# Performance work log

Measured on AMD Instinct MI355X. Metric: run time of the kernel, lower is better.

Reference implementation:

```python
import jax, jax.numpy as jnp
import numpy as np

T, B, N = 512, 256, 128


def setup_inputs() -> dict:
    key = jax.random.key(0)
    k1, k2, k3, k4, k5, k6 = jax.random.split(key, 6)
    emit = jax.random.normal(k1, (T, B, N), dtype=jnp.float32)
    target = jax.random.randint(k2, (T, B), 0, N)
    # prefix-true mask from random lengths in [1, T]
    lengths = jax.random.randint(k3, (B,), 1, T + 1)
    mask = jnp.arange(T)[:, None] < lengths[None, :]
    std = (1.0 / N) ** 0.5
    trans = jax.random.normal(k4, (N, N), dtype=jnp.float32) * std
    strans = jax.random.normal(k5, (N,), dtype=jnp.float32) * std
    etrans = jax.random.normal(k6, (N,), dtype=jnp.float32) * std
    return {"emit": emit, "target": target, "mask": mask,
            "trans": trans, "strans": strans, "etrans": etrans}


def _logZ(emit, mask, trans, strans, etrans):
    alpha0 = strans + emit[0]  # (B, N)

    def step(alpha, xs):
        e_t, m_t = xs  # (B, N), (B,)
        # scores[b, j] = logsumexp_i(alpha[b, i] + trans[i, j] + e_t[b, j])
        scores = jax.scipy.special.logsumexp(
            alpha[:, :, None] + trans[None, :, :] + e_t[:, None, :], axis=1)
        alpha = jnp.where(m_t[:, None], scores, alpha)
        return alpha, None

    alpha, _ = jax.lax.scan(step, alpha0, (emit[1:], mask[1:]))
    return jax.scipy.special.logsumexp(alpha + etrans, axis=1).sum()


def _score(emit, target, mask, trans, strans, etrans):
    Tn, Bn, _ = emit.shape
    # emission scores of gold tags: (T, B)
    sc = jnp.take_along_axis(emit, target[:, :, None], axis=2)[..., 0]
    # transition scores between consecutive gold tags
    sc = sc.at[1:].add(trans[target[:-1], target[1:]])
    score = jnp.sum(jnp.where(mask, sc, jnp.float32(0.0)))
    ends = mask.astype(jnp.int32).sum(axis=0) - 1  # (B,)
    score = score + strans[target[0]].sum()
    score = score + etrans[target[ends, jnp.arange(Bn)]].sum()
    return score


def reference(emit, target, mask, trans, strans, etrans):
    Bn = emit.shape[1]
    logZ = _logZ(emit, mask, trans, strans, etrans)
    score = _score(emit, target, mask, trans, strans, etrans)
    return (logZ - score) / Bn
```

## Files before the change

### kernel.cpp

```cpp
#include <hip/hip_runtime.h>

#define TT 512
#define BB 256
#define NN 128
#define MW 16
#define NWG (BB / MW)
#define STH 144

#define LENS_OFF 256
#define AF_OFF 2048
#define CF_OFF (AF_OFF + BB * NN * 4)
#define BU_OFF (CF_OFF + 1024)
#define CB_OFF (BU_OFF + BB * NN * 4)
#define WS_NEED ((size_t)CB_OFF + 1024)

typedef __attribute__((ext_vector_type(8))) short short8_t;
typedef __attribute__((ext_vector_type(4))) float f32x4;

__device__ __forceinline__ unsigned short f2bf(float f) {
  unsigned u = __float_as_uint(f);
  return (unsigned short)((u + 0x7FFF + ((u >> 16) & 1)) >> 16);
}
__device__ __forceinline__ float bf2f(unsigned short h) {
  return __uint_as_float(((unsigned)h) << 16);
}
__device__ __forceinline__ int orig_j(int p) {
  return 32 * (p >> 5) + 16 * (p & 1) + ((p >> 1) & 15);
}
__device__ __forceinline__ unsigned pk_bf16(float a, float b) {
  unsigned r;
  asm("v_cvt_pk_bf16_f32 %0, %1, %2" : "=v"(r) : "v"(a), "v"(b));
  return r;
}

#define BARRIER_LGKM() \
  asm volatile("s_waitcnt lgkmcnt(0)\n\ts_barrier" ::: "memory")

template <bool FWD>
__device__ __forceinline__ void step_one(
    int T_, bool NORM, const float* __restrict__ emit,
    unsigned short (&sVg)[2][MW * STH], int (&nrmg)[2][MW], int& nb,
    int (&cloc)[4], const int (&lm1)[4], const int (&off8)[8],
    float (&RL)[8], const float (&RO)[8], float (&xv)[8],
    const short8_t (&eB)[4][2], float eet0, float eet1, int w, int c, int qd,
    bool nwriter) {
  const int POUT = T_ & 1, PIN = POUT ^ 1;
  {
    int tl = FWD ? (T_ + 2 < TT ? T_ + 2 : TT - 1) : (T_ - 2 > 0 ? T_ - 2 : 0);
    const size_t gb = (size_t)tl * (BB * NN);
#pragma unroll
    for (int i = 0; i < 8; ++i) RL[i] = emit[gb + off8[i]];
  }
  const short8_t A0 = *(const short8_t*)&sVg[PIN][c * STH + 0 + qd * 8];
  const short8_t A1 = *(const short8_t*)&sVg[PIN][c * STH + 32 + qd * 8];
  const short8_t A2 = *(const short8_t*)&sVg[PIN][c * STH + 64 + qd * 8];
  const short8_t A3 = *(const short8_t*)&sVg[PIN][c * STH + 96 + qd * 8];
  f32x4 p0 = {0.f, 0.f, 0.f, 0.f}, q0 = {0.f, 0.f, 0.f, 0.f};
  f32x4 p1 = {0.f, 0.f, 0.f, 0.f}, q1 = {0.f, 0.f, 0.f, 0.f};
  p0 = __builtin_amdgcn_mfma_f32_16x16x32_bf16(A0, eB[0][0], p0, 0, 0, 0);
  p1 = __builtin_amdgcn_mfma_f32_16x16x32_bf16(A0, eB[0][1], p1, 0, 0, 0);
  q0 = __builtin_amdgcn_mfma_f32_16x16x32_bf16(A2, eB[2][0], q0, 0, 0, 0);
  q1 = __builtin_amdgcn_mfma_f32_16x16x32_bf16(A2, eB[2][1], q1, 0, 0, 0);
  p0 = __builtin_amdgcn_mfma_f32_16x16x32_bf16(A1, eB[1][0], p0, 0, 0, 0);
  p1 = __builtin_amdgcn_mfma_f32_16x16x32_bf16(A1, eB[1][1], p1, 0, 0, 0);
  q0 = __builtin_amdgcn_mfma_f32_16x16x32_bf16(A3, eB[3][0], q0, 0, 0, 0);
  q1 = __builtin_amdgcn_mfma_f32_16x16x32_bf16(A3, eB[3][1], q1, 0, 0, 0);
  const f32x4 ac0 = p0 + q0;
  const f32x4 ac1 = p1 + q1;

  if (NORM) {
    const int4 nr = *(const int4*)&nrmg[nb][4 * qd];
    const int nA[4] = {nr.x, nr.y, nr.z, nr.w};
    int nnw[4];
#pragma unroll
    for (int r_ = 0; r_ < 4; ++r_) {
      float v0, v1;
      if (FWD) {
        v0 = ldexpf(ac0[r_] * xv[2 * r_], -nA[r_]);
        v1 = ldexpf(ac1[r_] * xv[2 * r_ + 1], -nA[r_]);
        if (T_ <= lm1[r_]) {
          *(unsigned*)&sVg[POUT][(4 * qd + r_) * STH + 32 * w + 2 * c] =
              pk_bf16(v0, v1);
          cloc[r_] += nA[r_];
        }
      } else {
        const bool isact = (T_ == lm1[r_]);
        v0 = isact ? xv[2 * r_] * eet0 : ldexpf(ac0[r_] * xv[2 * r_], -nA[r_]);
        v1 = isact ? xv[2 * r_ + 1] * eet1
                   : ldexpf(ac1[r_] * xv[2 * r_ + 1], -nA[r_]);
        if (T_ <= lm1[r_]) {
          *(unsigned*)&sVg[POUT][(4 * qd + r_) * STH + 32 * w + 2 * c] =
              pk_bf16(v0, v1);
          cloc[r_] = isact ? 0 : cloc[r_] + nA[r_];
        }
      }
      nnw[r_] = ((int)((__float_as_uint(v0) >> 23) & 0xFF)) - 120;
    }
    if (nwriter)
      *(int4*)&nrmg[nb ^ 1][4 * qd] = make_int4(nnw[0], nnw[1], nnw[2], nnw[3]);
    nb ^= 1;
  } else {
#pragma unroll
    for (int r_ = 0; r_ < 4; ++r_) {
      float v0, v1;
      if (FWD) {
        v0 = ac0[r_] * xv[2 * r_];
        v1 = ac1[r_] * xv[2 * r_ + 1];
        if (T_ <= lm1[r_]) {
          *(unsigned*)&sVg[POUT][(4 * qd + r_) * STH + 32 * w + 2 * c] =
              pk_bf16(v0, v1);
        }
      } else {
        const bool isact = (T_ == lm1[r_]);
        v0 = isact ? xv[2 * r_] * eet0 : ac0[r_] * xv[2 * r_];
        v1 = isact ? xv[2 * r_ + 1] * eet1 : ac1[r_] * xv[2 * r_ + 1];
        if (T_ <= lm1[r_]) {
          *(unsigned*)&sVg[POUT][(4 * qd + r_) * STH + 32 * w + 2 * c] =
              pk_bf16(v0, v1);
          cloc[r_] = isact ? 0 : cloc[r_];
        }
      }
    }
  }
#pragma unroll
  for (int i = 0; i < 8; ++i) xv[i] = __expf(RO[i]);
}

__global__ __launch_bounds__(256, 1) void crf_fb5(
    const float* __restrict__ emit, const int* __restrict__ target,
    const void* __restrict__ maskp, const float* __restrict__ trans,
    const float* __restrict__ strans, const float* __restrict__ etrans,
    float* __restrict__ ws, int* __restrict__ lens, float* __restrict__ AF,
    int* __restrict__ CF, float* __restrict__ BU, int* __restrict__ CB) {
  __shared__ __align__(16) unsigned short sV[2][MW * STH];
  __shared__ __align__(16) int nrm[2][MW];
  __shared__ __align__(16) int sC[MW];
  __shared__ int slen[MW];
  __shared__ int smax_s;
  __shared__ float rf[4];

  const int bid = blockIdx.x;
  const unsigned char* mk8 = (const unsigned char*)maskp;
  const int* mk32 = (const int*)maskp;
  const bool is_u8 = (mk8[1] != 0);

  if (bid >= 32) {
    const int b = threadIdx.x;
    const int t = bid - 32;
    int m = is_u8 ? (mk8[t * BB + b] != 0) : (mk32[t * BB + b] != 0);
    float v = 0.f;
    if (m) {
      int tg = target[t * BB + b];
      v = emit[((size_t)t * BB + b) * NN + tg];
      v += (t > 0) ? trans[target[(t - 1) * BB + b] * NN + tg] : strans[tg];
      int mn = (t + 1 < TT) ? (is_u8 ? (mk8[(t + 1) * BB + b] != 0)
                                     : (mk32[(t + 1) * BB + b] != 0))
                            : 0;
      if (!mn) {
        v += etrans[tg];
        lens[b] = t + 1;
      }
    }
#pragma unroll
    for (int off = 32; off; off >>= 1) v += __shfl_down(v, off, 64);
    if ((b & 63) == 0) rf[b >> 6] = v;
    __syncthreads();
    if (b == 0) atomicAdd(&ws[1], rf[0] + rf[1] + rf[2] + rf[3]);
    return;
  }

  const int tid = threadIdx.x;
  const bool bwd = (bid >= NWG);
  const int g = bwd ? bid - NWG : bid;
  const int bg = g * MW;
  const int w = tid >> 6, l = tid & 63, c = l & 15, qd = l >> 4;

  if (tid == 0) smax_s = 0;
  __syncthreads();
  if (tid < MW) {
    const int b = bg + tid;
    int len = 1;
#pragma unroll
    for (int st = 256; st; st >>= 1) {
      int t2 = len + st;
      if (t2 <= TT) {
        bool mv = is_u8 ? (mk8[(size_t)(t2 - 1) * BB + b] != 0)
                        : (mk32[(size_t)(t2 - 1) * BB + b] != 0);
        if (mv) len = t2;
      }
    }
    slen[tid] = len;
    atomicMax(&smax_s, len);
  }

  short8_t eB[4][2];
#pragma unroll
  for (int kt = 0; kt < 4; ++kt)
#pragma unroll
    for (int u = 0; u < 2; ++u)
#pragma unroll
      for (int jj = 0; jj < 8; ++jj) {
        int kp = kt * 32 + qd * 8 + jj;
        int a_ = orig_j(kp);
        int b_ = 32 * w + 16 * u + c;
        float tv = bwd ? trans[b_ * NN + a_] : trans[a_ * NN + b_];
        eB[kt][u][jj] = (short)f2bf(__expf(tv));
      }
  const float eet0 = __expf(etrans[32 * w + c]);
  const float eet1 = __expf(etrans[32 * w + 16 + c]);

  {
    const int m = tid & 15;
    const int pbase = (tid >> 4) * 8;
    if (!bwd) {
      const int b = bg + m;
#pragma unroll
      for (int pp = 0; pp < 8; ++pp) {
        int p = pbase + pp;
        int j = orig_j(p);
        float v = __expf(strans[j] + emit[(size_t)b * NN + j]);
        sV[0][m * STH + p] = f2bf(v);
        if (p == 0)
          nrm[0][m] = ((int)((__float_as_uint(v) >> 23) & 0xFF)) - 120;
      }
    } else {
#pragma unroll
      for (int pp = 0; pp < 8; ++pp) {
        int p = pbase + pp;
        sV[0][m * STH + p] = 0x3F80;
        sV[1][m * STH + p] = 0x3F80;
        if (p == 0) { nrm[0][m] = 0; nrm[1][m] = 0; }
      }
    }
  }
  __syncthreads();
  const int smax = smax_s;
  int lm1[4];
#pragma unroll
  for (int r = 0; r < 4; ++r) lm1[r] = slen[4 * qd + r] - 1;

  int cloc[4] = {0, 0, 0, 0};
  int nb = 0;
  const bool nwriter = (w == 0 && c == 0);

  int off8[8];
#pragma unroll
  for (int r = 0; r < 4; ++r)
#pragma unroll
    for (int u = 0; u < 2; ++u)
      off8[r * 2 + u] = (bg + 4 * qd + r) * NN + 32 * w + 16 * u + c;

  int NIT, T0;
  if (!bwd) {
    const int LmaxF = (smax < 258) ? smax : 258;
    NIT = LmaxF - 1;
    T0 = 1;
  } else {
    NIT = (smax >= 259) ? smax - 258 : 0;
    T0 = smax - 1;
  }

  if (NIT > 0) {
    float ra[8], rb[8], xv[8];
    {
      const int a0 = T0;
      const int a1 = bwd ? (T0 - 1 > 0 ? T0 - 1 : 0)
                         : (T0 + 1 < TT ? T0 + 1 : TT - 1);
#pragma unroll
      for (int i = 0; i < 8; ++i) {
        ra[i] = emit[(size_t)a0 * (BB * NN) + off8[i]];
        rb[i] = emit[(size_t)a1 * (BB * NN) + off8[i]];
      }
#pragma unroll
      for (int i = 0; i < 8; ++i) xv[i] = __expf(ra[i]);
    }
    if (!bwd) {
      int it = 0;
      for (; it + 2 <= NIT; it += 2) {
        step_one<true>(T0 + it, false, emit, sV, nrm, nb, cloc, lm1, off8, ra,
                       rb, xv, eB, eet0, eet1, w, c, qd, nwriter);
        BARRIER_LGKM();
        step_one<true>(T0 + it + 1, true, emit, sV, nrm, nb, cloc, lm1, off8,
                       rb, ra, xv, eB, eet0, eet1, w, c, qd, nwriter);
        BARRIER_LGKM();
      }
      if (it < NIT) {
        step_one<true>(T0 + it, false, emit, sV, nrm, nb, cloc, lm1, off8, ra,
                       rb, xv, eB, eet0, eet1, w, c, qd, nwriter);
        BARRIER_LGKM();
      }
    } else {
      int it = 0;
      for (; it + 2 <= NIT; it += 2) {
        step_one<false>(T0 - it, false, emit, sV, nrm, nb, cloc, lm1, off8, ra,
                        rb, xv, eB, eet0, eet1, w, c, qd, nwriter);
        BARRIER_LGKM();
        step_one<false>(T0 - it - 1, true, emit, sV, nrm, nb, cloc, lm1, off8,
                        rb, ra, xv, eB, eet0, eet1, w, c, qd, nwriter);
        BARRIER_LGKM();
      }
      if (it < NIT) {
        step_one<false>(T0 - it, false, emit, sV, nrm, nb, cloc, lm1, off8, ra,
                        rb, xv, eB, eet0, eet1, w, c, qd, nwriter);
        BARRIER_LGKM();
      }
    }
  }

  if (nwriter)
    *(int4*)&sC[4 * qd] = make_int4(cloc[0], cloc[1], cloc[2], cloc[3]);
  __syncthreads();
  {
    const int m = tid >> 4, i16 = tid & 15;
    if (!bwd) {
      int nf = slen[m] - 1;
      if (nf > 257) nf = 257;
      const int pf = nf & 1;
#pragma unroll
      for (int pp = 0; pp < 8; ++pp) {
        int p = i16 * 8 + pp;
        AF[(size_t)(bg + m) * NN + p] = bf2f(sV[pf][m * STH + p]);
      }
      if (i16 == 0) CF[bg + m] = sC[m];
    } else {
#pragma unroll
      for (int pp = 0; pp < 8; ++pp) {
        int p = i16 * 8 + pp;
        BU[(size_t)(bg + m) * NN + p] = bf2f(sV[0][m * STH + p]);
      }
      if (i16 == 0) CB[bg + m] = sC[m];
    }
  }
}

__global__ __launch_bounds__(256) void crf_comb(
    const float* __restrict__ trans, const float* __restrict__ etrans,
    const int* __restrict__ lens, const float* __restrict__ AF,
    const int* __restrict__ CF, const float* __restrict__ BU,
    const int* __restrict__ CB, float* __restrict__ ws,
    float* __restrict__ out) {
  __shared__ __align__(16) unsigned short sU[MW * STH];
  __shared__ float sRed[4][MW][2];
  __shared__ int slen[MW];
  const int tid = threadIdx.x;
  const int w = tid >> 6, l = tid & 63, c = l & 15, qd = l >> 4;
  const int g = blockIdx.x, bg = g * MW;

  if (tid < MW) slen[tid] = lens[bg + tid];
  {
    const int m = tid & 15, pbase = (tid >> 4) * 8;
#pragma unroll
    for (int pp = 0; pp < 8; ++pp) {
      int p = pbase + pp;
      sU[m * STH + p] = f2bf(BU[(size_t)(bg + m) * NN + p]);
    }
  }
  short8_t eB[4][2];
#pragma unroll
  for (int kt = 0; kt < 4; ++kt)
#pragma unroll
    for (int u = 0; u < 2; ++u)
#pragma unroll
      for (int jj = 0; jj < 8; ++jj) {
        int kp = kt * 32 + qd * 8 + jj;
        int a_ = orig_j(kp);
        int b_ = 32 * w + 16 * u + c;
        eB[kt][u][jj] = (short)f2bf(__expf(trans[b_ * NN + a_]));
      }
  const float eet0 = __expf(etrans[32 * w + c]);
  const float eet1 = __expf(etrans[32 * w + 16 + c]);
  __syncthreads();

  const short8_t A0 = *(const short8_t*)&sU[c * STH + 0 + qd * 8];
  const short8_t A1 = *(const short8_t*)&sU[c * STH + 32 + qd * 8];
  const short8_t A2 = *(const short8_t*)&sU[c * STH + 64 + qd * 8];
  const short8_t A3 = *(const short8_t*)&sU[c * STH + 96 + qd * 8];
  f32x4 ac0 = {0.f, 0.f, 0.f, 0.f}, ac1 = {0.f, 0.f, 0.f, 0.f};
  ac0 = __builtin_amdgcn_mfma_f32_16x16x32_bf16(A0, eB[0][0], ac0, 0, 0, 0);
  ac1 = __builtin_amdgcn_mfma_f32_16x16x32_bf16(A0, eB[0][1], ac1, 0, 0, 0);
  ac0 = __builtin_amdgcn_mfma_f32_16x16x32_bf16(A1, eB[1][0], ac0, 0, 0, 0);
  ac1 = __builtin_amdgcn_mfma_f32_16x16x32_bf16(A1, eB[1][1], ac1, 0, 0, 0);
  ac0 = __builtin_amdgcn_mfma_f32_16x16x32_bf16(A2, eB[2][0], ac0, 0, 0, 0);
  ac1 = __builtin_amdgcn_mfma_f32_16x16x32_bf16(A2, eB[2][1], ac1, 0, 0, 0);
  ac0 = __builtin_amdgcn_mfma_f32_16x16x32_bf16(A3, eB[3][0], ac0, 0, 0, 0);
  ac1 = __builtin_amdgcn_mfma_f32_16x16x32_bf16(A3, eB[3][1], ac1, 0, 0, 0);

#pragma unroll
  for (int r_ = 0; r_ < 4; ++r_) {
    float a0 = AF[(size_t)(bg + 4 * qd + r_) * NN + 32 * w + 2 * c];
    float a1 = AF[(size_t)(bg + 4 * qd + r_) * NN + 32 * w + 2 * c + 1];
    float dB = a0 * ac0[r_] + a1 * ac1[r_];
    float dA = a0 * eet0 + a1 * eet1;
#pragma unroll
    for (int mk = 1; mk < 16; mk <<= 1) {
      dB += __shfl_xor(dB, mk, 64);
      dA += __shfl_xor(dA, mk, 64);
    }
    if (c == 0) {
      sRed[w][4 * qd + r_][0] = dB;
      sRed[w][4 * qd + r_][1] = dA;
    }
  }
  __syncthreads();
  if (tid < MW) {
    float DB = sRed[0][tid][0] + sRed[1][tid][0] + sRed[2][tid][0] + sRed[3][tid][0];
    float DA = sRed[0][tid][1] + sRed[1][tid][1] + sRed[2][tid][1] + sRed[3][tid][1];
    const int len = slen[tid];
    const float LN2 = 0.6931471805599453f;
    float logZ;
    if (len >= 259)
      logZ = LN2 * (float)(CF[bg + tid] + CB[bg + tid]) + __logf(DB);
    else
      logZ = LN2 * (float)CF[bg + tid] + __logf(DA);
    atomicAdd(&ws[0], logZ);
  }
  __syncthreads();
  if (tid == 0) {
    __threadfence();
    unsigned old = atomicAdd((unsigned*)ws + 3, 1u);
    if (old == NWG - 1) {
      float zz = atomicAdd(&ws[0], 0.f);
      float ss = atomicAdd(&ws[1], 0.f);
      out[0] = (zz - ss) * (1.0f / (float)BB);
    }
  }
}

__global__ __launch_bounds__(256, 1) void crf_fused_fb(
    const float* __restrict__ emit, const int* __restrict__ target,
    const void* __restrict__ maskp, const float* __restrict__ trans,
    const float* __restrict__ strans, const float* __restrict__ etrans,
    float* __restrict__ ws, float* __restrict__ out) {
  __shared__ __align__(16) unsigned short sV[2][MW * STH];
  __shared__ __align__(16) int nrm[2][MW];
  __shared__ __align__(16) int sC[MW];
  __shared__ int slen[MW];
  __shared__ float sscore;
  __shared__ int smax;

  const int tid = threadIdx.x;
  const int w = tid >> 6;
  const int l = tid & 63;
  const int c = l & 15;
  const int qd = l >> 4;
  const int bg = blockIdx.x * MW;

  if (tid < MW) slen[tid] = 0;
  if (tid == 0) { sscore = 0.f; smax = 0; }
  __syncthreads();

  const unsigned char* mk8 = (const unsigned char*)maskp;
  const int* mk32 = (const int*)maskp;
  const bool is_u8 = (mk8[1] != 0);
  {
    const int mi = tid & 15;
    const int b = bg + mi;
    const int t0 = (tid >> 4) * 32;
    int cnt = 0;
    float sc = 0.f;
    for (int s = 0; s < 32; ++s) {
      int t = t0 + s;
      int m = is_u8 ? (mk8[t * BB + b] != 0) : (mk32[t * BB + b] != 0);
      if (m) {
        cnt++;
        int tg = target[t * BB + b];
        float v = emit[((size_t)t * BB + b) * NN + tg];
        v += (t > 0) ? trans[target[(t - 1) * BB + b] * NN + tg] : strans[tg];
        int mn = (t + 1 < TT) ? (is_u8 ? (mk8[(t + 1) * BB + b] != 0)
                                       : (mk32[(t + 1) * BB + b] != 0))
                              : 0;
        if (!mn) v += etrans[tg];
        sc += v;
      }
    }
    atomicAdd(&slen[mi], cnt);
    atomicAdd(&sscore, sc);
  }

  short8_t eB[4][2];
#pragma unroll
  for (int kt = 0; kt < 4; ++kt)
#pragma unroll
    for (int u = 0; u < 2; ++u)
#pragma unroll
      for (int jj = 0; jj < 8; ++jj) {
        int kp = kt * 32 + qd * 8 + jj;
        int i = orig_j(kp);
        int j = 32 * w + 16 * u + c;
        eB[kt][u][jj] = (short)f2bf(__expf(trans[i * NN + j]));
      }

  {
    const int m = tid & 15;
    const int b = bg + m;
    const int pbase = (tid >> 4) * 8;
#pragma unroll
    for (int pp = 0; pp < 8; ++pp) {
      int p = pbase + pp;
      int j = orig_j(p);
      float v = __expf(strans[j] + emit[(size_t)b * NN + j]);
      sV[0][m * STH + p] = f2bf(v);
      if (p == 0)
        nrm[0][m] = ((int)((__float_as_uint(v) >> 23) & 0xFF)) - 120;
    }
  }
  __syncthreads();

  if (tid < MW) atomicMax(&smax, slen[tid]);
  if (tid == 0) atomicAdd(&ws[1], sscore);
  __syncthreads();
  const int Lmax = smax;
  int lenr[4];
#pragma unroll
  for (int r = 0; r < 4; ++r) lenr[r] = slen[4 * qd + r];

  int off8[8];
#pragma unroll
  for (int r = 0; r < 4; ++r)
#pragma unroll
    for (int u = 0; u < 2; ++u)
      off8[r * 2 + u] = (bg + 4 * qd + r) * NN + 32 * w + 16 * u + c;

  float ra[8], rb[8], xv[8];
  {
#pragma unroll
    for (int i = 0; i < 8; ++i) ra[i] = emit[(size_t)1 * BB * NN + off8[i]];
#pragma unroll
    for (int i = 0; i < 8; ++i) rb[i] = emit[(size_t)2 * BB * NN + off8[i]];
#pragma unroll
    for (int i = 0; i < 8; ++i) xv[i] = __expf(ra[i]);
  }
  int cloc[4] = {0, 0, 0, 0};
  const bool nwriter = (w == 0 && c == 0);

#define CRF_STEP(T_, PIN, POUT, RL, RO)                                       \
  do {                                                                        \
    int tl = ((T_) + 2 < TT) ? (T_) + 2 : TT - 1;                             \
    const size_t gbase = (size_t)tl * (BB * NN);                              \
    _Pragma("unroll") for (int i_ = 0; i_ < 8; ++i_)                          \
        RL[i_] = emit[gbase + off8[i_]];                                      \
    const short8_t A0 = *(const short8_t*)&sV[PIN][c * STH + 0 + qd * 8];     \
    const short8_t A1 = *(const short8_t*)&sV[PIN][c * STH + 32 + qd * 8];    \
    const short8_t A2 = *(const short8_t*)&sV[PIN][c * STH + 64 + qd * 8];    \
    const short8_t A3 = *(const short8_t*)&sV[PIN][c * STH + 96 + qd * 8];    \
    const int4 nr = *(const int4*)&nrm[PIN][4 * qd];                          \
    f32x4 ac0 = {0.f, 0.f, 0.f, 0.f}, ac1 = {0.f, 0.f, 0.f, 0.f};             \
    ac0 = __builtin_amdgcn_mfma_f32_16x16x32_bf16(A0, eB[0][0], ac0, 0, 0, 0);\
    ac1 = __builtin_amdgcn_mfma_f32_16x16x32_bf16(A0, eB[0][1], ac1, 0, 0, 0);\
    ac0 = __builtin_amdgcn_mfma_f32_16x16x32_bf16(A1, eB[1][0], ac0, 0, 0, 0);\
    ac1 = __builtin_amdgcn_mfma_f32_16x16x32_bf16(A1, eB[1][1], ac1, 0, 0, 0);\
    ac0 = __builtin_amdgcn_mfma_f32_16x16x32_bf16(A2, eB[2][0], ac0, 0, 0, 0);\
    ac1 = __builtin_amdgcn_mfma_f32_16x16x32_bf16(A2, eB[2][1], ac1, 0, 0, 0);\
    ac0 = __builtin_amdgcn_mfma_f32_16x16x32_bf16(A3, eB[3][0], ac0, 0, 0, 0);\
    ac1 = __builtin_amdgcn_mfma_f32_16x16x32_bf16(A3, eB[3][1], ac1, 0, 0, 0);\
    const int nA[4] = {nr.x, nr.y, nr.z, nr.w};                               \
    int nnw[4];                                                               \
    _Pragma("unroll") for (int r_ = 0; r_ < 4; ++r_) {                        \
      float y0 = ac0[r_] * xv[2 * r_];                                        \
      float y1 = ac1[r_] * xv[2 * r_ + 1];                                    \
      float v0 = ldexpf(y0, -nA[r_]);                                         \
      float v1 = ldexpf(y1, -nA[r_]);                                         \
      if ((T_) < lenr[r_]) {                                                  \
        unsigned pk = (unsigned)f2bf(v0) | ((unsigned)f2bf(v1) << 16);        \
        *(unsigned*)&sV[POUT][(4 * qd + r_) * STH + 32 * w + 2 * c] = pk;     \
        cloc[r_] += nA[r_];                                                   \
      }                                                                       \
      nnw[r_] = ((int)((__float_as_uint(v0) >> 23) & 0xFF)) - 120;            \
    }                                                                         \
    if (nwriter)                                                              \
      *(int4*)&nrm[POUT][4 * qd] = make_int4(nnw[0], nnw[1], nnw[2], nnw[3]); \
    _Pragma("unroll") for (int i_ = 0; i_ < 8; ++i_)                          \
        xv[i_] = __expf(RO[i_]);                                              \
    __syncthreads();                                                          \
  } while (0)

  for (int t = 1; t < Lmax; t += 2) {
    CRF_STEP(t, 0, 1, ra, rb);
    if (t + 1 < Lmax) {
      CRF_STEP(t + 1, 1, 0, rb, ra);
    }
  }
#undef CRF_STEP

  if (nwriter) *(int4*)&sC[4 * qd] = make_int4(cloc[0], cloc[1], cloc[2], cloc[3]);
  __syncthreads();
  {
    const int m = tid >> 4, i16 = tid & 15;
    const int pb = (slen[m] - 1) & 1;
    float s = 0.f;
#pragma unroll
    for (int pp = 0; pp < 8; ++pp) {
      int p = i16 * 8 + pp;
      int j = orig_j(p);
      s += bf2f(sV[pb][m * STH + p]) * __expf(etrans[j]);
    }
    s += __shfl_xor(s, 1, 64);
    s += __shfl_xor(s, 2, 64);
    s += __shfl_xor(s, 4, 64);
    s += __shfl_xor(s, 8, 64);
    if (i16 == 0)
      atomicAdd(&ws[0], (float)sC[m] * 0.69314718f + __logf(s));
  }
  __syncthreads();
  if (tid == 0) {
    __threadfence();
    unsigned old = atomicAdd((unsigned*)ws + 3, 1u);
    if (old == NWG - 1) {
      float zz = atomicAdd(&ws[0], 0.f);
      float ss = atomicAdd(&ws[1], 0.f);
      out[0] = (zz - ss) * (1.0f / (float)BB);
    }
  }
}

extern "C" void kernel_launch(void* const* d_in, const int* in_sizes, int n_in,
                              void* d_out, int out_size, void* d_ws, size_t ws_size,
                              hipStream_t stream) {
  const float* emit = (const float*)d_in[0];
  const int* target = (const int*)d_in[1];
  const void* mask = (const void*)d_in[2];
  const float* trans = (const float*)d_in[3];
  const float* strans = (const float*)d_in[4];
  const float* etrans = (const float*)d_in[5];
  float* ws = (float*)d_ws;
  float* out = (float*)d_out;

  hipMemsetAsync(d_ws, 0, 16, stream);
  if (ws_size >= WS_NEED) {
    int* lens = (int*)((char*)d_ws + LENS_OFF);
    float* AF = (float*)((char*)d_ws + AF_OFF);
    int* CF = (int*)((char*)d_ws + CF_OFF);
    float* BU = (float*)((char*)d_ws + BU_OFF);
    int* CB = (int*)((char*)d_ws + CB_OFF);
    crf_fb5<<<32 + TT, 256, 0, stream>>>(emit, target, mask, trans, strans,
                                         etrans, ws, lens, AF, CF, BU, CB);
    crf_comb<<<NWG, 256, 0, stream>>>(trans, etrans, lens, AF, CF, BU, CB, ws,
                                      out);
  } else {
    crf_fused_fb<<<NWG, 256, 0, stream>>>(emit, target, mask, trans, strans,
                                          etrans, ws, out);
  }
}
```

Measured before the change: 230.9 us.

## Fuse combine kernel into main kernel via spin-wait counter, renormalize every fourth step

The separate combine kernel is folded into the main kernel as extra blocks. They precompute exp(trans) and then spin on a global counter until all producer and forward/backward blocks finish, which removes one kernel launch and its gap. The exponential normalization now runs on every fourth step instead of every second. The exp of the next emission is moved between the MFMAs and the epilogue, using double-buffered x registers so it overlaps with the matrix ops. The spin-wait relies on the consumer blocks being co-resident with the producers, which risks deadlock or idle waiting, and less frequent renormalization raises the risk of bf16 overflow or underflow.

Result: slower. 240.7 us (+4.2%).

```diff
diff --git a/kernel.cpp b/kernel.cpp
--- a/kernel.cpp
+++ b/kernel.cpp
@@ -6,6 +6,8 @@
 #define MW 16
 #define NWG (BB / MW)
 #define STH 144
+#define NPROD (32 + TT)
+#define GRID (NPROD + NWG)
 
 #define LENS_OFF 256
 #define AF_OFF 2048
@@ -41,9 +43,9 @@
     int T_, bool NORM, const float* __restrict__ emit,
     unsigned short (&sVg)[2][MW * STH], int (&nrmg)[2][MW], int& nb,
     int (&cloc)[4], const int (&lm1)[4], const int (&off8)[8],
-    float (&RL)[8], const float (&RO)[8], float (&xv)[8],
-    const short8_t (&eB)[4][2], float eet0, float eet1, int w, int c, int qd,
-    bool nwriter) {
+    float (&RL)[8], const float (&RO)[8], const float (&XU)[8],
+    float (&XF)[8], const short8_t (&eB)[4][2], float eet0, float eet1,
+    int w, int c, int qd, bool nwriter) {
   const int POUT = T_ & 1, PIN = POUT ^ 1;
   {
     int tl = FWD ? (T_ + 2 < TT ? T_ + 2 : TT - 1) : (T_ - 2 > 0 ? T_ - 2 : 0);
@@ -65,6 +67,8 @@
   p1 = __builtin_amdgcn_mfma_f32_16x16x32_bf16(A1, eB[1][1], p1, 0, 0, 0);
   q0 = __builtin_amdgcn_mfma_f32_16x16x32_bf16(A3, eB[3][0], q0, 0, 0, 0);
   q1 = __builtin_amdgcn_mfma_f32_16x16x32_bf16(A3, eB[3][1], q1, 0, 0, 0);
+#pragma unroll
+  for (int i = 0; i < 8; ++i) XF[i] = __expf(RO[i]);
   const f32x4 ac0 = p0 + q0;
   const f32x4 ac1 = p1 + q1;
 
@@ -76,8 +80,8 @@
     for (int r_ = 0; r_ < 4; ++r_) {
       float v0, v1;
       if (FWD) {
-        v0 = ldexpf(ac0[r_] * xv[2 * r_], -nA[r_]);
-        v1 = ldexpf(ac1[r_] * xv[2 * r_ + 1], -nA[r_]);
+        v0 = ldexpf(ac0[r_] * XU[2 * r_], -nA[r_]);
+        v1 = ldexpf(ac1[r_] * XU[2 * r_ + 1], -nA[r_]);
         if (T_ <= lm1[r_]) {
           *(unsigned*)&sVg[POUT][(4 * qd + r_) * STH + 32 * w + 2 * c] =
               pk_bf16(v0, v1);
@@ -85,9 +89,9 @@
         }
       } else {
         const bool isact = (T_ == lm1[r_]);
-        v0 = isact ? xv[2 * r_] * eet0 : ldexpf(ac0[r_] * xv[2 * r_], -nA[r_]);
-        v1 = isact ? xv[2 * r_ + 1] * eet1
-                   : ldexpf(ac1[r_] * xv[2 * r_ + 1], -nA[r_]);
+        v0 = isact ? XU[2 * r_] * eet0 : ldexpf(ac0[r_] * XU[2 * r_], -nA[r_]);
+        v1 = isact ? XU[2 * r_ + 1] * eet1
+                   : ldexpf(ac1[r_] * XU[2 * r_ + 1], -nA[r_]);
         if (T_ <= lm1[r_]) {
           *(unsigned*)&sVg[POUT][(4 * qd + r_) * STH + 32 * w + 2 * c] =
               pk_bf16(v0, v1);
@@ -104,16 +108,16 @@
     for (int r_ = 0; r_ < 4; ++r_) {
       float v0, v1;
       if (FWD) {
-        v0 = ac0[r_] * xv[2 * r_];
-        v1 = ac1[r_] * xv[2 * r_ + 1];
+        v0 = ac0[r_] * XU[2 * r_];
+        v1 = ac1[r_] * XU[2 * r_ + 1];
         if (T_ <= lm1[r_]) {
           *(unsigned*)&sVg[POUT][(4 * qd + r_) * STH + 32 * w + 2 * c] =
               pk_bf16(v0, v1);
         }
       } else {
         const bool isact = (T_ == lm1[r_]);
-        v0 = isact ? xv[2 * r_] * eet0 : ac0[r_] * xv[2 * r_];
-        v1 = isact ? xv[2 * r_ + 1] * eet1 : ac1[r_] * xv[2 * r_ + 1];
+        v0 = isact ? XU[2 * r_] * eet0 : ac0[r_] * XU[2 * r_];
+        v1 = isact ? XU[2 * r_ + 1] * eet1 : ac1[r_] * XU[2 * r_ + 1];
         if (T_ <= lm1[r_]) {
           *(unsigned*)&sVg[POUT][(4 * qd + r_) * STH + 32 * w + 2 * c] =
               pk_bf16(v0, v1);
@@ -122,30 +126,33 @@
       }
     }
   }
-#pragma unroll
-  for (int i = 0; i < 8; ++i) xv[i] = __expf(RO[i]);
-}
-
-__global__ __launch_bounds__(256, 1) void crf_fb5(
+}
+
+__global__ __launch_bounds__(256, 1) void crf_fb6(
     const float* __restrict__ emit, const int* __restrict__ target,
     const void* __restrict__ maskp, const float* __restrict__ trans,
     const float* __restrict__ strans, const float* __restrict__ etrans,
     float* __restrict__ ws, int* __restrict__ lens, float* __restrict__ AF,
-    int* __restrict__ CF, float* __restrict__ BU, int* __restrict__ CB) {
+    int* __restrict__ CF, float* __restrict__ BU, int* __restrict__ CB,
+    float* __restrict__ out) {
   __shared__ __align__(16) unsigned short sV[2][MW * STH];
   __shared__ __align__(16) int nrm[2][MW];
   __shared__ __align__(16) int sC[MW];
   __shared__ int slen[MW];
   __shared__ int smax_s;
   __shared__ float rf[4];
+  __shared__ __align__(16) unsigned short sU[MW * STH];
+  __shared__ float sRed[4][MW][2];
 
   const int bid = blockIdx.x;
+  const int tid = threadIdx.x;
   const unsigned char* mk8 = (const unsigned char*)maskp;
   const int* mk32 = (const int*)maskp;
   const bool is_u8 = (mk8[1] != 0);
-
-  if (bid >= 32) {
-    const int b = threadIdx.x;
+  unsigned* const cnt = (unsigned*)ws + 2;
+
+  if (bid >= 32 && bid < NPROD) {
+    const int b = tid;
     const int t = bid - 32;
     int m = is_u8 ? (mk8[t * BB + b] != 0) : (mk32[t * BB + b] != 0);
     float v = 0.f;
@@ -165,11 +172,108 @@
     for (int off = 32; off; off >>= 1) v += __shfl_down(v, off, 64);
     if ((b & 63) == 0) rf[b >> 6] = v;
     __syncthreads();
-    if (b == 0) atomicAdd(&ws[1], rf[0] + rf[1] + rf[2] + rf[3]);
+    if (b == 0) {
+      atomicAdd(&ws[1], rf[0] + rf[1] + rf[2] + rf[3]);
+      __threadfence();
+      atomicAdd(cnt, 1u);
+    }
     return;
   }
 
-  const int tid = threadIdx.x;
+  if (bid >= NPROD) {
+    const int w = tid >> 6, l = tid & 63, c = l & 15, qd = l >> 4;
+    const int g = bid - NPROD, bg = g * MW;
+
+    short8_t eB[4][2];
+#pragma unroll
+    for (int kt = 0; kt < 4; ++kt)
+#pragma unroll
+      for (int u = 0; u < 2; ++u)
+#pragma unroll
+        for (int jj = 0; jj < 8; ++jj) {
+          int kp = kt * 32 + qd * 8 + jj;
+          int a_ = orig_j(kp);
+          int b_ = 32 * w + 16 * u + c;
+          eB[kt][u][jj] = (short)f2bf(__expf(trans[b_ * NN + a_]));
+        }
+    const float eet0 = __expf(etrans[32 * w + c]);
+    const float eet1 = __expf(etrans[32 * w + 16 + c]);
+
+    if (tid == 0) {
+      while (atomicAdd(cnt, 0u) < (unsigned)NPROD) __builtin_amdgcn_s_sleep(32);
+    }
+    __syncthreads();
+    __threadfence();
+
+    if (tid < MW) slen[tid] = lens[bg + tid];
+    {
+      const int m = tid & 15, pbase = (tid >> 4) * 8;
+#pragma unroll
+      for (int pp = 0; pp < 8; ++pp) {
+        int p = pbase + pp;
+        sU[m * STH + p] = f2bf(BU[(size_t)(bg + m) * NN + p]);
+      }
+    }
+    __syncthreads();
+
+    const short8_t A0 = *(const short8_t*)&sU[c * STH + 0 + qd * 8];
+    const short8_t A1 = *(const short8_t*)&sU[c * STH + 32 + qd * 8];
+    const short8_t A2 = *(const short8_t*)&sU[c * STH + 64 + qd * 8];
+    const short8_t A3 = *(const short8_t*)&sU[c * STH + 96 + qd * 8];
+    f32x4 ac0 = {0.f, 0.f, 0.f, 0.f}, ac1 = {0.f, 0.f, 0.f, 0.f};
+    ac0 = __builtin_amdgcn_mfma_f32_16x16x32_bf16(A0, eB[0][0], ac0, 0, 0, 0);
+    ac1 = __builtin_amdgcn_mfma_f32_16x16x32_bf16(A0, eB[0][1], ac1, 0, 0, 0);
+    ac0 = __builtin_amdgcn_mfma_f32_16x16x32_bf16(A1, eB[1][0], ac0, 0, 0, 0);
+    ac1 = __builtin_amdgcn_mfma_f32_16x16x32_bf16(A1, eB[1][1], ac1, 0, 0, 0);
+    ac0 = __builtin_amdgcn_mfma_f32_16x16x32_bf16(A2, eB[2][0], ac0, 0, 0, 0);
+    ac1 = __builtin_amdgcn_mfma_f32_16x16x32_bf16(A2, eB[2][1], ac1, 0, 0, 0);
+    ac0 = __builtin_amdgcn_mfma_f32_16x16x32_bf16(A3, eB[3][0], ac0, 0, 0, 0);
+    ac1 = __builtin_amdgcn_mfma_f32_16x16x32_bf16(A3, eB[3][1], ac1, 0, 0, 0);
+
+#pragma unroll
+    for (int r_ = 0; r_ < 4; ++r_) {
+      float a0 = AF[(size_t)(bg + 4 * qd + r_) * NN + 32 * w + 2 * c];
+      float a1 = AF[(size_t)(bg + 4 * qd + r_) * NN + 32 * w + 2 * c + 1];
+      float dB = a0 * ac0[r_] + a1 * ac1[r_];
+      float dA = a0 * eet0 + a1 * eet1;
+#pragma unroll
+      for (int mk = 1; mk < 16; mk <<= 1) {
+        dB += __shfl_xor(dB, mk, 64);
+        dA += __shfl_xor(dA, mk, 64);
+      }
+      if (c == 0) {
+        sRed[w][4 * qd + r_][0] = dB;
+        sRed[w][4 * qd + r_][1] = dA;
+      }
+    }
+    __syncthreads();
+    if (tid < MW) {
+      float DB =
+          sRed[0][tid][0] + sRed[1][tid][0] + sRed[2][tid][0] + sRed[3][tid][0];
+      float DA =
+          sRed[0][tid][1] + sRed[1][tid][1] + sRed[2][tid][1] + sRed[3][tid][1];
+      const int len = slen[tid];
+      const float LN2 = 0.6931471805599453f;
+      float logZ;
+      if (len >= 259)
+        logZ = LN2 * (float)(CF[bg + tid] + CB[bg + tid]) + __logf(DB);
+      else
+        logZ = LN2 * (float)CF[bg + tid] + __logf(DA);
+      atomicAdd(&ws[0], logZ);
+    }
+    __syncthreads();
+    if (tid == 0) {
+      __threadfence();
+      unsigned old = atomicAdd((unsigned*)ws + 3, 1u);
+      if (old == NWG - 1) {
+        float zz = atomicAdd(&ws[0], 0.f);
+        float ss = atomicAdd(&ws[1], 0.f);
+        out[0] = (zz - ss) * (1.0f / (float)BB);
+      }
+    }
+    return;
+  }
+
   const bool bwd = (bid >= NWG);
   const int g = bwd ? bid - NWG : bid;
   const int bg = g * MW;
@@ -261,48 +365,49 @@
   }
 
   if (NIT > 0) {
-    float ra[8], rb[8], xv[8];
+    float ra[8], rb[8], x0[8], x1[8];
     {
-      const int a0 = T0;
       const int a1 = bwd ? (T0 - 1 > 0 ? T0 - 1 : 0)
                          : (T0 + 1 < TT ? T0 + 1 : TT - 1);
 #pragma unroll
       for (int i = 0; i < 8; ++i) {
-        ra[i] = emit[(size_t)a0 * (BB * NN) + off8[i]];
+        ra[i] = emit[(size_t)T0 * (BB * NN) + off8[i]];
         rb[i] = emit[(size_t)a1 * (BB * NN) + off8[i]];
       }
 #pragma unroll
-      for (int i = 0; i < 8; ++i) xv[i] = __expf(ra[i]);
+      for (int i = 0; i < 8; ++i) x0[i] = __expf(ra[i]);
     }
     if (!bwd) {
-      int it = 0;
-      for (; it + 2 <= NIT; it += 2) {
-        step_one<true>(T0 + it, false, emit, sV, nrm, nb, cloc, lm1, off8, ra,
-                       rb, xv, eB, eet0, eet1, w, c, qd, nwriter);
-        BARRIER_LGKM();
-        step_one<true>(T0 + it + 1, true, emit, sV, nrm, nb, cloc, lm1, off8,
-                       rb, ra, xv, eB, eet0, eet1, w, c, qd, nwriter);
-        BARRIER_LGKM();
-      }
-      if (it < NIT) {
-        step_one<true>(T0 + it, false, emit, sV, nrm, nb, cloc, lm1, off8, ra,
-                       rb, xv, eB, eet0, eet1, w, c, qd, nwriter);
-        BARRIER_LGKM();
+      for (int itb = 0; itb < NIT; itb += 4) {
+#pragma unroll
+        for (int k = 0; k < 4; ++k) {
+          const int it = itb + k;
+          if (it >= NIT) break;
+          if ((k & 1) == 0)
+            step_one<true>(T0 + it, k == 3, emit, sV, nrm, nb, cloc, lm1, off8,
+                           ra, rb, x0, x1, eB, eet0, eet1, w, c, qd, nwriter);
+          else
+            step_one<true>(T0 + it, k == 3, emit, sV, nrm, nb, cloc, lm1, off8,
+                           rb, ra, x1, x0, eB, eet0, eet1, w, c, qd, nwriter);
+          BARRIER_LGKM();
+        }
       }
     } else {
-      int it = 0;
-      for (; it + 2 <= NIT; it += 2) {
-        step_one<false>(T0 - it, false, emit, sV, nrm, nb, cloc, lm1, off8, ra,
-                        rb, xv, eB, eet0, eet1, w, c, qd, nwriter);
-        BARRIER_LGKM();
-        step_one<false>(T0 - it - 1, true, emit, sV, nrm, nb, cloc, lm1, off8,
-                        rb, ra, xv, eB, eet0, eet1, w, c, qd, nwriter);
-        BARRIER_LGKM();
-      }
-      if (it < NIT) {
-        step_one<false>(T0 - it, false, emit, sV, nrm, nb, cloc, lm1, off8, ra,
-                        rb, xv, eB, eet0, eet1, w, c, qd, nwriter);
-        BARRIER_LGKM();
+      for (int itb = 0; itb < NIT; itb += 4) {
+#pragma unroll
+        for (int k = 0; k < 4; ++k) {
+          const int it = itb + k;
+          if (it >= NIT) break;
+          if ((k & 1) == 0)
+            step_one<false>(T0 - it, k == 3, emit, sV, nrm, nb, cloc, lm1,
+                            off8, ra, rb, x0, x1, eB, eet0, eet1, w, c, qd,
+                            nwriter);
+          else
+            step_one<false>(T0 - it, k == 3, emit, sV, nrm, nb, cloc, lm1,
+                            off8, rb, ra, x1, x0, eB, eet0, eet1, w, c, qd,
+                            nwriter);
+          BARRIER_LGKM();
+        }
       }
     }
   }
@@ -331,98 +436,10 @@
       if (i16 == 0) CB[bg + m] = sC[m];
     }
   }
-}
-
-__global__ __launch_bounds__(256) void crf_comb(
-    const float* __restrict__ trans, const float* __restrict__ etrans,
-    const int* __restrict__ lens, const float* __restrict__ AF,
-    const int* __restrict__ CF, const float* __restrict__ BU,
-    const int* __restrict__ CB, float* __restrict__ ws,
-    float* __restrict__ out) {
-  __shared__ __align__(16) unsigned short sU[MW * STH];
-  __shared__ float sRed[4][MW][2];
-  __shared__ int slen[MW];
-  const int tid = threadIdx.x;
-  const int w = tid >> 6, l = tid & 63, c = l & 15, qd = l >> 4;
-  const int g = blockIdx.x, bg = g * MW;
-
-  if (tid < MW) slen[tid] = lens[bg + tid];
-  {
-    const int m = tid & 15, pbase = (tid >> 4) * 8;
-#pragma unroll
-    for (int pp = 0; pp < 8; ++pp) {
-      int p = pbase + pp;
-      sU[m * STH + p] = f2bf(BU[(size_t)(bg + m) * NN + p]);
-    }
-  }
-  short8_t eB[4][2];
-#pragma unroll
-  for (int kt = 0; kt < 4; ++kt)
-#pragma unroll
-    for (int u = 0; u < 2; ++u)
-#pragma unroll
-      for (int jj = 0; jj < 8; ++jj) {
-        int kp = kt * 32 + qd * 8 + jj;
-        int a_ = orig_j(kp);
-        int b_ = 32 * w + 16 * u + c;
-        eB[kt][u][jj] = (short)f2bf(__expf(trans[b_ * NN + a_]));
-      }
-  const float eet0 = __expf(etrans[32 * w + c]);
-  const float eet1 = __expf(etrans[32 * w + 16 + c]);
-  __syncthreads();
-
-  const short8_t A0 = *(const short8_t*)&sU[c * STH + 0 + qd * 8];
-  const short8_t A1 = *(const short8_t*)&sU[c * STH + 32 + qd * 8];
-  const short8_t A2 = *(const short8_t*)&sU[c * STH + 64 + qd * 8];
-  const short8_t A3 = *(const short8_t*)&sU[c * STH + 96 + qd * 8];
-  f32x4 ac0 = {0.f, 0.f, 0.f, 0.f}, ac1 = {0.f, 0.f, 0.f, 0.f};
-  ac0 = __builtin_amdgcn_mfma_f32_16x16x32_bf16(A0, eB[0][0], ac0, 0, 0, 0);
-  ac1 = __builtin_amdgcn_mfma_f32_16x16x32_bf16(A0, eB[0][1], ac1, 0, 0, 0);
-  ac0 = __builtin_amdgcn_mfma_f32_16x16x32_bf16(A1, eB[1][0], ac0, 0, 0, 0);
-  ac1 = __builtin_amdgcn_mfma_f32_16x16x32_bf16(A1, eB[1][1], ac1, 0, 0, 0);
-  ac0 = __builtin_amdgcn_mfma_f32_16x16x32_bf16(A2, eB[2][0], ac0, 0, 0, 0);
-  ac1 = __builtin_amdgcn_mfma_f32_16x16x32_bf16(A2, eB[2][1], ac1, 0, 0, 0);
-  ac0 = __builtin_amdgcn_mfma_f32_16x16x32_bf16(A3, eB[3][0], ac0, 0, 0, 0);
-  ac1 = __builtin_amdgcn_mfma_f32_16x16x32_bf16(A3, eB[3][1], ac1, 0, 0, 0);
-
-#pragma unroll
-  for (int r_ = 0; r_ < 4; ++r_) {
-    float a0 = AF[(size_t)(bg + 4 * qd + r_) * NN + 32 * w + 2 * c];
-    float a1 = AF[(size_t)(bg + 4 * qd + r_) * NN + 32 * w + 2 * c + 1];
-    float dB = a0 * ac0[r_] + a1 * ac1[r_];
-    float dA = a0 * eet0 + a1 * eet1;
-#pragma unroll
-    for (int mk = 1; mk < 16; mk <<= 1) {
-      dB += __shfl_xor(dB, mk, 64);
-      dA += __shfl_xor(dA, mk, 64);
-    }
-    if (c == 0) {
-      sRed[w][4 * qd + r_][0] = dB;
-      sRed[w][4 * qd + r_][1] = dA;
-    }
-  }
-  __syncthreads();
-  if (tid < MW) {
-    float DB = sRed[0][tid][0] + sRed[1][tid][0] + sRed[2][tid][0] + sRed[3][tid][0];
-    float DA = sRed[0][tid][1] + sRed[1][tid][1] + sRed[2][tid][1] + sRed[3][tid][1];
-    const int len = slen[tid];
-    const float LN2 = 0.6931471805599453f;
-    float logZ;
-    if (len >= 259)
-      logZ = LN2 * (float)(CF[bg + tid] + CB[bg + tid]) + __logf(DB);
-    else
-      logZ = LN2 * (float)CF[bg + tid] + __logf(DA);
-    atomicAdd(&ws[0], logZ);
-  }
   __syncthreads();
   if (tid == 0) {
     __threadfence();
-    unsigned old = atomicAdd((unsigned*)ws + 3, 1u);
-    if (old == NWG - 1) {
-      float zz = atomicAdd(&ws[0], 0.f);
-      float ss = atomicAdd(&ws[1], 0.f);
-      out[0] = (zz - ss) * (1.0f / (float)BB);
-    }
+    atomicAdd(cnt, 1u);
   }
 }
 
@@ -632,10 +649,8 @@
     int* CF = (int*)((char*)d_ws + CF_OFF);
     float* BU = (float*)((char*)d_ws + BU_OFF);
     int* CB = (int*)((char*)d_ws + CB_OFF);
-    crf_fb5<<<32 + TT, 256, 0, stream>>>(emit, target, mask, trans, strans,
-                                         etrans, ws, lens, AF, CF, BU, CB);
-    crf_comb<<<NWG, 256, 0, stream>>>(trans, etrans, lens, AF, CF, BU, CB, ws,
-                                      out);
+    crf_fb6<<<GRID, 256, 0, stream>>>(emit, target, mask, trans, strans,
+                                      etrans, ws, lens, AF, CF, BU, CB, out);
   } else {
     crf_fused_fb<<<NWG, 256, 0, stream>>>(emit, target, mask, trans, strans,
                                           etrans, ws, out);
```

## Fuse combine kernel into forward-backward kernel via atomic counter spin-wait

Applied to the files above, without the earlier changes.

Folds the separate combine kernel into the main kernel as 16 extra trailing blocks. Those blocks precompute exp(trans) fragments, then spin on a global atomic counter until all 544 producer blocks (forward/backward and gold-score blocks) have signalled completion, and only then run the combine step. This removes one kernel launch and its launch gap. It relies on the consumer blocks being scheduled without starving the producers, which could deadlock if residency were limited, and the spinning blocks occupy CUs while they wait.

Measured after the change: 244.0 us. +5.7%, slower.

```diff
diff --git a/kernel.cpp b/kernel.cpp
--- a/kernel.cpp
+++ b/kernel.cpp
@@ -6,6 +6,8 @@
 #define MW 16
 #define NWG (BB / MW)
 #define STH 144
+#define NPROD (32 + TT)
+#define GRID (NPROD + NWG)
 
 #define LENS_OFF 256
 #define AF_OFF 2048
@@ -126,26 +128,31 @@
   for (int i = 0; i < 8; ++i) xv[i] = __expf(RO[i]);
 }
 
-__global__ __launch_bounds__(256, 1) void crf_fb5(
+__global__ __launch_bounds__(256, 1) void crf_fb7(
     const float* __restrict__ emit, const int* __restrict__ target,
     const void* __restrict__ maskp, const float* __restrict__ trans,
     const float* __restrict__ strans, const float* __restrict__ etrans,
     float* __restrict__ ws, int* __restrict__ lens, float* __restrict__ AF,
-    int* __restrict__ CF, float* __restrict__ BU, int* __restrict__ CB) {
+    int* __restrict__ CF, float* __restrict__ BU, int* __restrict__ CB,
+    float* __restrict__ out) {
   __shared__ __align__(16) unsigned short sV[2][MW * STH];
   __shared__ __align__(16) int nrm[2][MW];
   __shared__ __align__(16) int sC[MW];
   __shared__ int slen[MW];
   __shared__ int smax_s;
   __shared__ float rf[4];
+  __shared__ __align__(16) unsigned short sU[MW * STH];
+  __shared__ float sRed[4][MW][2];
 
   const int bid = blockIdx.x;
+  const int tid = threadIdx.x;
   const unsigned char* mk8 = (const unsigned char*)maskp;
   const int* mk32 = (const int*)maskp;
   const bool is_u8 = (mk8[1] != 0);
-
-  if (bid >= 32) {
-    const int b = threadIdx.x;
+  unsigned* const cnt = (unsigned*)ws + 2;
+
+  if (bid >= 32 && bid < NPROD) {
+    const int b = tid;
     const int t = bid - 32;
     int m = is_u8 ? (mk8[t * BB + b] != 0) : (mk32[t * BB + b] != 0);
     float v = 0.f;
@@ -165,11 +172,108 @@
     for (int off = 32; off; off >>= 1) v += __shfl_down(v, off, 64);
     if ((b & 63) == 0) rf[b >> 6] = v;
     __syncthreads();
-    if (b == 0) atomicAdd(&ws[1], rf[0] + rf[1] + rf[2] + rf[3]);
+    if (b == 0) {
+      atomicAdd(&ws[1], rf[0] + rf[1] + rf[2] + rf[3]);
+      __threadfence();
+      atomicAdd(cnt, 1u);
+    }
     return;
   }
 
-  const int tid = threadIdx.x;
+  if (bid >= NPROD) {
+    const int w = tid >> 6, l = tid & 63, c = l & 15, qd = l >> 4;
+    const int g = bid - NPROD, bg = g * MW;
+
+    short8_t eB[4][2];
+#pragma unroll
+    for (int kt = 0; kt < 4; ++kt)
+#pragma unroll
+      for (int u = 0; u < 2; ++u)
+#pragma unroll
+        for (int jj = 0; jj < 8; ++jj) {
+          int kp = kt * 32 + qd * 8 + jj;
+          int a_ = orig_j(kp);
+          int b_ = 32 * w + 16 * u + c;
+          eB[kt][u][jj] = (short)f2bf(__expf(trans[b_ * NN + a_]));
+        }
+    const float eet0 = __expf(etrans[32 * w + c]);
+    const float eet1 = __expf(etrans[32 * w + 16 + c]);
+
+    if (tid == 0) {
+      while (atomicAdd(cnt, 0u) < (unsigned)NPROD) __builtin_amdgcn_s_sleep(32);
+    }
+    __syncthreads();
+    __threadfence();
+
+    if (tid < MW) slen[tid] = lens[bg + tid];
+    {
+      const int m = tid & 15, pbase = (tid >> 4) * 8;
+#pragma unroll
+      for (int pp = 0; pp < 8; ++pp) {
+        int p = pbase + pp;
+        sU[m * STH + p] = f2bf(BU[(size_t)(bg + m) * NN + p]);
+      }
+    }
+    __syncthreads();
+
+    const short8_t A0 = *(const short8_t*)&sU[c * STH + 0 + qd * 8];
+    const short8_t A1 = *(const short8_t*)&sU[c * STH + 32 + qd * 8];
+    const short8_t A2 = *(const short8_t*)&sU[c * STH + 64 + qd * 8];
+    const short8_t A3 = *(const short8_t*)&sU[c * STH + 96 + qd * 8];
+    f32x4 ac0 = {0.f, 0.f, 0.f, 0.f}, ac1 = {0.f, 0.f, 0.f, 0.f};
+    ac0 = __builtin_amdgcn_mfma_f32_16x16x32_bf16(A0, eB[0][0], ac0, 0, 0, 0);
+    ac1 = __builtin_amdgcn_mfma_f32_16x16x32_bf16(A0, eB[0][1], ac1, 0, 0, 0);
+    ac0 = __builtin_amdgcn_mfma_f32_16x16x32_bf16(A1, eB[1][0], ac0, 0, 0, 0);
+    ac1 = __builtin_amdgcn_mfma_f32_16x16x32_bf16(A1, eB[1][1], ac1, 0, 0, 0);
+    ac0 = __builtin_amdgcn_mfma_f32_16x16x32_bf16(A2, eB[2][0], ac0, 0, 0, 0);
+    ac1 = __builtin_amdgcn_mfma_f32_16x16x32_bf16(A2, eB[2][1], ac1, 0, 0, 0);
+    ac0 = __builtin_amdgcn_mfma_f32_16x16x32_bf16(A3, eB[3][0], ac0, 0, 0, 0);
+    ac1 = __builtin_amdgcn_mfma_f32_16x16x32_bf16(A3, eB[3][1], ac1, 0, 0, 0);
+
+#pragma unroll
+    for (int r_ = 0; r_ < 4; ++r_) {
+      float a0 = AF[(size_t)(bg + 4 * qd + r_) * NN + 32 * w + 2 * c];
+      float a1 = AF[(size_t)(bg + 4 * qd + r_) * NN + 32 * w + 2 * c + 1];
+      float dB = a0 * ac0[r_] + a1 * ac1[r_];
+      float dA = a0 * eet0 + a1 * eet1;
+#pragma unroll
+      for (int mk = 1; mk < 16; mk <<= 1) {
+        dB += __shfl_xor(dB, mk, 64);
+        dA += __shfl_xor(dA, mk, 64);
+      }
+      if (c == 0) {
+        sRed[w][4 * qd + r_][0] = dB;
+        sRed[w][4 * qd + r_][1] = dA;
+      }
+    }
+    __syncthreads();
+    if (tid < MW) {
+      float DB =
+          sRed[0][tid][0] + sRed[1][tid][0] + sRed[2][tid][0] + sRed[3][tid][0];
+      float DA =
+          sRed[0][tid][1] + sRed[1][tid][1] + sRed[2][tid][1] + sRed[3][tid][1];
+      const int len = slen[tid];
+      const float LN2 = 0.6931471805599453f;
+      float logZ;
+      if (len >= 259)
+        logZ = LN2 * (float)(CF[bg + tid] + CB[bg + tid]) + __logf(DB);
+      else
+        logZ = LN2 * (float)CF[bg + tid] + __logf(DA);
+      atomicAdd(&ws[0], logZ);
+    }
+    __syncthreads();
+    if (tid == 0) {
+      __threadfence();
+      unsigned old = atomicAdd((unsigned*)ws + 3, 1u);
+      if (old == NWG - 1) {
+        float zz = atomicAdd(&ws[0], 0.f);
+        float ss = atomicAdd(&ws[1], 0.f);
+        out[0] = (zz - ss) * (1.0f / (float)BB);
+      }
+    }
+    return;
+  }
+
   const bool bwd = (bid >= NWG);
   const int g = bwd ? bid - NWG : bid;
   const int bg = g * MW;
@@ -263,12 +367,11 @@
   if (NIT > 0) {
     float ra[8], rb[8], xv[8];
     {
-      const int a0 = T0;
       const int a1 = bwd ? (T0 - 1 > 0 ? T0 - 1 : 0)
                          : (T0 + 1 < TT ? T0 + 1 : TT - 1);
 #pragma unroll
       for (int i = 0; i < 8; ++i) {
-        ra[i] = emit[(size_t)a0 * (BB * NN) + off8[i]];
+        ra[i] = emit[(size_t)T0 * (BB * NN) + off8[i]];
         rb[i] = emit[(size_t)a1 * (BB * NN) + off8[i]];
       }
 #pragma unroll
@@ -331,98 +434,10 @@
       if (i16 == 0) CB[bg + m] = sC[m];
     }
   }
-}
-
-__global__ __launch_bounds__(256) void crf_comb(
-    const float* __restrict__ trans, const float* __restrict__ etrans,
-    const int* __restrict__ lens, const float* __restrict__ AF,
-    const int* __restrict__ CF, const float* __restrict__ BU,
-    const int* __restrict__ CB, float* __restrict__ ws,
-    float* __restrict__ out) {
-  __shared__ __align__(16) unsigned short sU[MW * STH];
-  __shared__ float sRed[4][MW][2];
-  __shared__ int slen[MW];
-  const int tid = threadIdx.x;
-  const int w = tid >> 6, l = tid & 63, c = l & 15, qd = l >> 4;
-  const int g = blockIdx.x, bg = g * MW;
-
-  if (tid < MW) slen[tid] = lens[bg + tid];
-  {
-    const int m = tid & 15, pbase = (tid >> 4) * 8;
-#pragma unroll
-    for (int pp = 0; pp < 8; ++pp) {
-      int p = pbase + pp;
-      sU[m * STH + p] = f2bf(BU[(size_t)(bg + m) * NN + p]);
-    }
-  }
-  short8_t eB[4][2];
-#pragma unroll
-  for (int kt = 0; kt < 4; ++kt)
-#pragma unroll
-    for (int u = 0; u < 2; ++u)
-#pragma unroll
-      for (int jj = 0; jj < 8; ++jj) {
-        int kp = kt * 32 + qd * 8 + jj;
-        int a_ = orig_j(kp);
-        int b_ = 32 * w + 16 * u + c;
-        eB[kt][u][jj] = (short)f2bf(__expf(trans[b_ * NN + a_]));
-      }
-  const float eet0 = __expf(etrans[32 * w + c]);
-  const float eet1 = __expf(etrans[32 * w + 16 + c]);
-  __syncthreads();
-
-  const short8_t A0 = *(const short8_t*)&sU[c * STH + 0 + qd * 8];
-  const short8_t A1 = *(const short8_t*)&sU[c * STH + 32 + qd * 8];
-  const short8_t A2 = *(const short8_t*)&sU[c * STH + 64 + qd * 8];
-  const short8_t A3 = *(const short8_t*)&sU[c * STH + 96 + qd * 8];
-  f32x4 ac0 = {0.f, 0.f, 0.f, 0.f}, ac1 = {0.f, 0.f, 0.f, 0.f};
-  ac0 = __builtin_amdgcn_mfma_f32_16x16x32_bf16(A0, eB[0][0], ac0, 0, 0, 0);
-  ac1 = __builtin_amdgcn_mfma_f32_16x16x32_bf16(A0, eB[0][1], ac1, 0, 0, 0);
-  ac0 = __builtin_amdgcn_mfma_f32_16x16x32_bf16(A1, eB[1][0], ac0, 0, 0, 0);
-  ac1 = __builtin_amdgcn_mfma_f32_16x16x32_bf16(A1, eB[1][1], ac1, 0, 0, 0);
-  ac0 = __builtin_amdgcn_mfma_f32_16x16x32_bf16(A2, eB[2][0], ac0, 0, 0, 0);
-  ac1 = __builtin_amdgcn_mfma_f32_16x16x32_bf16(A2, eB[2][1], ac1, 0, 0, 0);
-  ac0 = __builtin_amdgcn_mfma_f32_16x16x32_bf16(A3, eB[3][0], ac0, 0, 0, 0);
-  ac1 = __builtin_amdgcn_mfma_f32_16x16x32_bf16(A3, eB[3][1], ac1, 0, 0, 0);
-
-#pragma unroll
-  for (int r_ = 0; r_ < 4; ++r_) {
-    float a0 = AF[(size_t)(bg + 4 * qd + r_) * NN + 32 * w + 2 * c];
-    float a1 = AF[(size_t)(bg + 4 * qd + r_) * NN + 32 * w + 2 * c + 1];
-    float dB = a0 * ac0[r_] + a1 * ac1[r_];
-    float dA = a0 * eet0 + a1 * eet1;
-#pragma unroll
-    for (int mk = 1; mk < 16; mk <<= 1) {
-      dB += __shfl_xor(dB, mk, 64);
-      dA += __shfl_xor(dA, mk, 64);
-    }
-    if (c == 0) {
-      sRed[w][4 * qd + r_][0] = dB;
-      sRed[w][4 * qd + r_][1] = dA;
-    }
-  }
-  __syncthreads();
-  if (tid < MW) {
-    float DB = sRed[0][tid][0] + sRed[1][tid][0] + sRed[2][tid][0] + sRed[3][tid][0];
-    float DA = sRed[0][tid][1] + sRed[1][tid][1] + sRed[2][tid][1] + sRed[3][tid][1];
-    const int len = slen[tid];
-    const float LN2 = 0.6931471805599453f;
-    float logZ;
-    if (len >= 259)
-      logZ = LN2 * (float)(CF[bg + tid] + CB[bg + tid]) + __logf(DB);
-    else
-      logZ = LN2 * (float)CF[bg + tid] + __logf(DA);
-    atomicAdd(&ws[0], logZ);
-  }
   __syncthreads();
   if (tid == 0) {
     __threadfence();
-    unsigned old = atomicAdd((unsigned*)ws + 3, 1u);
-    if (old == NWG - 1) {
-      float zz = atomicAdd(&ws[0], 0.f);
-      float ss = atomicAdd(&ws[1], 0.f);
-      out[0] = (zz - ss) * (1.0f / (float)BB);
-    }
+    atomicAdd(cnt, 1u);
   }
 }
 
@@ -632,10 +647,8 @@
     int* CF = (int*)((char*)d_ws + CF_OFF);
     float* BU = (float*)((char*)d_ws + BU_OFF);
     int* CB = (int*)((char*)d_ws + CB_OFF);
-    crf_fb5<<<32 + TT, 256, 0, stream>>>(emit, target, mask, trans, strans,
-                                         etrans, ws, lens, AF, CF, BU, CB);
-    crf_comb<<<NWG, 256, 0, stream>>>(trans, etrans, lens, AF, CF, BU, CB, ws,
-                                      out);
+    crf_fb7<<<GRID, 256, 0, stream>>>(emit, target, mask, trans, strans,
+                                      etrans, ws, lens, AF, CF, BU, CB, out);
   } else {
     crf_fused_fb<<<NWG, 256, 0, stream>>>(emit, target, mask, trans, strans,
                                           etrans, ws, out);
```
